# Kernel optimization log

Hardware: AMD Instinct MI355X
Metric: run time of the kernel (lower is better)

The kernel has to match this reference:

```python
import jax, jax.numpy as jnp
import numpy as np

B, N, K, E, H, V = 128, 256, 4, 300, 150, 32000  # batch, nodes/tree, max children, embed, hidden, vocab
DELTA = 1.0


def setup_inputs() -> dict:
    key = jax.random.key(0)
    ks = jax.random.split(key, 8)
    query = jax.random.randint(ks[0], (B, N), 0, V, dtype=jnp.int32)
    pos = jax.random.randint(ks[1], (B, N), 0, V, dtype=jnp.int32)
    neg = jax.random.randint(ks[2], (B, N), 0, V, dtype=jnp.int32)
    # Complete K-ary tree over N nodes: children of node t are {K*t+1, ..., K*t+K} < N; root = node 0.
    ch = np.full((N, K), -1, dtype=np.int32)
    for t in range(N):
        for j in range(K):
            c = K * t + 1 + j
            if c < N:
                ch[t, j] = c
    children = jnp.asarray(ch)
    emb = jax.random.normal(ks[3], (V, E), dtype=jnp.float32) * 0.02
    W_iou = jax.random.normal(ks[4], (E, 3 * H), dtype=jnp.float32) * 0.05
    U_iou = jax.random.normal(ks[5], (H, 3 * H), dtype=jnp.float32) * 0.05
    b_iou = jnp.zeros((3 * H,), jnp.float32)
    W_f = jax.random.normal(ks[6], (E, H), dtype=jnp.float32) * 0.05
    U_f = jax.random.normal(ks[7], (H, H), dtype=jnp.float32) * 0.05
    b_f = jnp.zeros((H,), jnp.float32)
    return {"query": query, "pos": pos, "neg": neg, "children": children,
            "emb": emb, "W_iou": W_iou, "U_iou": U_iou, "b_iou": b_iou,
            "W_f": W_f, "U_f": U_f, "b_f": b_f}


def _childsum_treelstm(x, children, W_iou, U_iou, b_iou, W_f, U_f, b_f):
    """x: [B, N, E] node embeddings. Returns root (c, h): each [B, H]."""
    Bn, Nn, _ = x.shape
    Hh = U_f.shape[0]
    h0 = jnp.zeros((Bn, Nn, Hh), x.dtype)
    c0 = jnp.zeros((Bn, Nn, Hh), x.dtype)

    def step(carry, t):
        h_all, c_all = carry
        ch = children[t]                        # [K] child indices, -1 = padding
        mask = (ch >= 0)
        idx = jnp.where(mask, ch, 0)
        m = mask.astype(x.dtype)[None, :, None]  # [1, K, 1]
        h_k = h_all[:, idx] * m                 # [B, K, H]
        c_k = c_all[:, idx] * m
        h_sum = h_k.sum(axis=1)                 # child-sum h_tilde [B, H]
        x_t = x[:, t]                           # [B, E]
        iou = x_t @ W_iou + h_sum @ U_iou + b_iou
        i, o, u = jnp.split(iou, 3, axis=-1)
        i = jax.nn.sigmoid(i)
        o = jax.nn.sigmoid(o)
        u = jnp.tanh(u)
        # per-child forget gates: f_jk = sigmoid(W_f x_j + U_f h_k + b_f)
        f = jax.nn.sigmoid((x_t @ W_f + b_f)[:, None, :] + h_k @ U_f)  # [B, K, H]
        c_t = i * u + (f * c_k).sum(axis=1)     # c_k already masked
        h_t = o * jnp.tanh(c_t)
        return (h_all.at[:, t].set(h_t), c_all.at[:, t].set(c_t)), None

    # children have larger indices than parents -> process N-1 .. 0 (root last)
    (h_all, c_all), _ = jax.lax.scan(step, (h0, c0), jnp.arange(Nn - 1, -1, -1))
    return c_all[:, 0], h_all[:, 0]


def _cosine(a, b):
    num = (a * b).sum(-1)
    den = jnp.sqrt((a * a).sum(-1) * (b * b).sum(-1)) + 1e-8
    return num / den


def reference(query, pos, neg, children, emb, W_iou, U_iou, b_iou, W_f, U_f, b_f):
    qc, _ = _childsum_treelstm(emb[query], children, W_iou, U_iou, b_iou, W_f, U_f, b_f)
    pc, _ = _childsum_treelstm(emb[pos], children, W_iou, U_iou, b_iou, W_f, U_f, b_f)
    nc, _ = _childsum_treelstm(emb[neg], children, W_iou, U_iou, b_iou, W_f, U_f, b_f)
    a = _cosine(qc, pc)  # [B]
    b = _cosine(qc, nc)  # [B]
    return jax.nn.relu(DELTA - a + b)
```

## Files before the change

### kernel.cpp

```cpp
#include <hip/hip_runtime.h>
#include <hip/hip_bf16.h>

typedef short short8 __attribute__((ext_vector_type(8)));
typedef float floatx4 __attribute__((ext_vector_type(4)));
typedef unsigned short ushort;

#define Bb 128
#define Nn 256
#define Hh 150
#define HK 160
#define Vv 32000
#define NROW 384
#define NINT 64
#define ZROW (Vv + NROW * NINT)

__device__ __forceinline__ float sigf(float x) { return 1.0f / (1.0f + __expf(-x)); }
__device__ __forceinline__ float tanhf_(float x) { return 1.0f - 2.0f / (__expf(2.0f * x) + 1.0f); }
__device__ __forceinline__ float bf2f(ushort s) { union { float f; unsigned u; } v; v.u = ((unsigned)s) << 16; return v.f; }
__device__ __forceinline__ ushort f2bf(float f) { __hip_bfloat16 h = __float2bfloat16(f); return *(ushort*)&h; }

__global__ __launch_bounds__(256) void k_prep(
    const float* __restrict__ W_iou, const float* __restrict__ W_f,
    const float* __restrict__ U_iou, const float* __restrict__ U_f,
    const float* __restrict__ b_iou, const float* __restrict__ b_f,
    short* __restrict__ Wt, short* __restrict__ Uti, short* __restrict__ Utf,
    float* __restrict__ biasw, ushort* __restrict__ h_u, float* __restrict__ c_u)
{
    int idx = blockIdx.x * 256 + threadIdx.x;
    const int nWt = 640 * 320, nUi = 464 * 160, nUf = 160 * 160;
    if (idx < nWt) {
        int n = idx / 320, k = idx % 320;
        int seg = n / 160, cc = n % 160;
        float v = 0.f;
        if (k < 300 && cc < 150) {
            if (seg == 0)      v = W_iou[k * 450 + cc];
            else if (seg == 1) v = W_iou[k * 450 + 150 + cc];
            else if (seg == 2) v = W_iou[k * 450 + 300 + cc];
            else               v = W_f[k * 150 + cc];
        }
        Wt[idx] = (short)f2bf(v);
    } else if (idx < nWt + nUi) {
        int i2 = idx - nWt; int n = i2 / 160, k = i2 % 160;
        float v = (k < 150 && n < 450) ? U_iou[k * 450 + n] : 0.f;
        Uti[i2] = (short)f2bf(v);
    } else if (idx < nWt + nUi + nUf) {
        int i2 = idx - nWt - nUi; int n = i2 / 160, k = i2 % 160;
        float v = (k < 150) ? U_f[k * 150 + n] : 0.f;
        Utf[i2] = (short)f2bf(v);
    } else if (idx < nWt + nUi + nUf + 640) {
        int n = idx - nWt - nUi - nUf;
        int seg = n / 160, cc = n % 160;
        biasw[n] = (cc < 150) ? (seg < 3 ? b_iou[seg * 150 + cc] : b_f[cc]) : 0.f;
    } else if (idx < nWt + nUi + nUf + 640 + HK) {
        int k = idx - (nWt + nUi + nUf + 640);
        h_u[(long)ZROW * HK + k] = 0;
        c_u[(long)ZROW * HK + k] = 0.f;
    }
}

__global__ __launch_bounds__(256) void k_vproj(
    const float* __restrict__ emb, const short* __restrict__ Wt,
    const float* __restrict__ biasw, ushort* __restrict__ proj,
    ushort* __restrict__ h_u, float* __restrict__ c_u)
{
    __shared__ __align__(16) short As[32 * 328];
    __shared__ __align__(16) float Tc[4][32][20];
    __shared__ __align__(16) ushort Th[4][32][24];
    const int tid = threadIdx.x;
    const int v0 = blockIdx.x * 32;

    for (int i = tid; i < 32 * 80; i += 256) {
        int r = i / 80, q = i % 80, k0 = q * 4;
        short4 sv;
        if (k0 < 300) {
            float4 x = *(const float4*)(emb + (long)(v0 + r) * 300 + k0);
            sv.x = (short)f2bf(x.x); sv.y = (short)f2bf(x.y);
            sv.z = (short)f2bf(x.z); sv.w = (short)f2bf(x.w);
        } else sv = make_short4(0, 0, 0, 0);
        *(short4*)&As[r * 328 + k0] = sv;
    }
    __syncthreads();

    const int w = tid >> 6, lane = tid & 63;
    const int m = lane & 15, quad = lane >> 4, kq = quad * 8;

    short8 a0[10], a1[10];
    #pragma unroll
    for (int ks = 0; ks < 10; ks++) {
        a0[ks] = *(const short8*)&As[m * 328 + kq + ks * 32];
        a1[ks] = *(const short8*)&As[(16 + m) * 328 + kq + ks * 32];
    }

    for (int j = w; j < 10; j += 4) {
        int col = j * 16 + m;
        const short* bp = Wt + (long)col * 320 + kq;
        floatx4 acc[4][2];
        #pragma unroll
        for (int s = 0; s < 4; s++) { acc[s][0] = {0.f,0.f,0.f,0.f}; acc[s][1] = {0.f,0.f,0.f,0.f}; }
        #pragma unroll
        for (int ks = 0; ks < 10; ks++) {
            short8 b0 = *(const short8*)(bp + 0 * 160 * 320 + ks * 32);
            short8 b1 = *(const short8*)(bp + 1 * 160 * 320 + ks * 32);
            short8 b2 = *(const short8*)(bp + 2 * 160 * 320 + ks * 32);
            short8 b3 = *(const short8*)(bp + 3 * 160 * 320 + ks * 32);
            acc[0][0] = __builtin_amdgcn_mfma_f32_16x16x32_bf16(a0[ks], b0, acc[0][0], 0, 0, 0);
            acc[0][1] = __builtin_amdgcn_mfma_f32_16x16x32_bf16(a1[ks], b0, acc[0][1], 0, 0, 0);
            acc[1][0] = __builtin_amdgcn_mfma_f32_16x16x32_bf16(a0[ks], b1, acc[1][0], 0, 0, 0);
            acc[1][1] = __builtin_amdgcn_mfma_f32_16x16x32_bf16(a1[ks], b1, acc[1][1], 0, 0, 0);
            acc[2][0] = __builtin_amdgcn_mfma_f32_16x16x32_bf16(a0[ks], b2, acc[2][0], 0, 0, 0);
            acc[2][1] = __builtin_amdgcn_mfma_f32_16x16x32_bf16(a1[ks], b2, acc[2][1], 0, 0, 0);
            acc[3][0] = __builtin_amdgcn_mfma_f32_16x16x32_bf16(a0[ks], b3, acc[3][0], 0, 0, 0);
            acc[3][1] = __builtin_amdgcn_mfma_f32_16x16x32_bf16(a1[ks], b3, acc[3][1], 0, 0, 0);
        }

        float bias[4] = { biasw[col], biasw[160 + col], biasw[320 + col], biasw[480 + col] };
        float pre[4][2][4];
        #pragma unroll
        for (int s = 0; s < 4; s++)
            #pragma unroll
            for (int g = 0; g < 2; g++)
                #pragma unroll
                for (int reg = 0; reg < 4; reg++)
                    pre[s][g][reg] = acc[s][g][reg] + bias[s];

        long tbase = (long)(blockIdx.x * 10 + j) * 2048;
        #pragma unroll
        for (int s = 0; s < 4; s++)
            #pragma unroll
            for (int g = 0; g < 2; g++) {
                unsigned u0 = (unsigned)f2bf(pre[s][g][0]) | ((unsigned)f2bf(pre[s][g][1]) << 16);
                unsigned u1 = (unsigned)f2bf(pre[s][g][2]) | ((unsigned)f2bf(pre[s][g][3]) << 16);
                *(uint2*)(proj + tbase + s * 512 + g * 256 + lane * 4) = make_uint2(u0, u1);
            }

        #pragma unroll
        for (int g = 0; g < 2; g++)
            #pragma unroll
            for (int reg = 0; reg < 4; reg++) {
                float iv = sigf(pre[0][g][reg]);
                float ov = sigf(pre[1][g][reg]);
                float uv = tanhf_(pre[2][g][reg]);
                float cc = iv * uv;
                int rr = g * 16 + quad * 4 + reg;
                Tc[w][rr][m] = cc;
                Th[w][rr][m] = f2bf(ov * tanhf_(cc));
            }
        asm volatile("s_waitcnt lgkmcnt(0)" ::: "memory");
        {
            int row = lane >> 1, half = lane & 1;
            int4 hv = *(const int4*)&Th[w][row][half * 8];
            *(int4*)(h_u + (long)(v0 + row) * HK + j * 16 + half * 8) = hv;
            #pragma unroll
            for (int qq = half; qq < 4; qq += 2) {
                float4 cv4 = *(const float4*)&Tc[w][row][qq * 4];
                *(float4*)(c_u + (long)(v0 + row) * HK + j * 16 + qq * 4) = cv4;
            }
        }
        asm volatile("s_waitcnt lgkmcnt(0)" ::: "memory");
    }
}

__global__ __launch_bounds__(256) void k_level(
    int t0, int G,
    const int* __restrict__ tq, const int* __restrict__ tp, const int* __restrict__ tn,
    const int* __restrict__ children, const ushort* __restrict__ proj,
    const short* __restrict__ Uti, const short* __restrict__ Utf,
    ushort* __restrict__ h_u, float* __restrict__ c_u)
{
    __shared__ __align__(16) short As[5][16][168];
    __shared__ int idx_s[16][4];
    __shared__ int tok_s[16];

    const int tid = threadIdx.x;
    const int gi = blockIdx.x % G;
    const int rest = blockIdx.x / G;
    const int t = t0 + rest / 24;
    const int r0 = (rest % 24) * 16;

    if (tid < 64) {
        int r = tid >> 2, j = tid & 3;
        int rg = r0 + r, g = rg >> 7, b = rg & 127;
        const int* tok = (g == 0) ? tq : (g == 1 ? tp : tn);
        int ch = children[t * 4 + j];
        int idx;
        if (ch < 0)        idx = ZROW;
        else if (ch >= 64) idx = tok[b * Nn + ch];
        else               idx = Vv + rg * NINT + ch;
        idx_s[r][j] = idx;
        if (j == 0) tok_s[r] = tok[b * Nn + t];
    }
    __syncthreads();

    for (int i = tid; i < 16 * 20; i += 256) {
        int r = i / 20, k0 = (i % 20) * 8;
        int4 v0 = *(const int4*)(h_u + (long)idx_s[r][0] * HK + k0);
        int4 v1 = *(const int4*)(h_u + (long)idx_s[r][1] * HK + k0);
        int4 v2 = *(const int4*)(h_u + (long)idx_s[r][2] * HK + k0);
        int4 v3 = *(const int4*)(h_u + (long)idx_s[r][3] * HK + k0);
        *(int4*)&As[1][r][k0] = v0;
        *(int4*)&As[2][r][k0] = v1;
        *(int4*)&As[3][r][k0] = v2;
        *(int4*)&As[4][r][k0] = v3;
        ushort s[8];
        const ushort* p0 = (const ushort*)&v0; const ushort* p1 = (const ushort*)&v1;
        const ushort* p2 = (const ushort*)&v2; const ushort* p3 = (const ushort*)&v3;
        #pragma unroll
        for (int e = 0; e < 8; e++)
            s[e] = f2bf(bf2f(p0[e]) + bf2f(p1[e]) + bf2f(p2[e]) + bf2f(p3[e]));
        *(int4*)&As[0][r][k0] = *(int4*)s;
    }
    __syncthreads();

    const int w = tid >> 6, lane = tid & 63;
    const int m = lane & 15, kq = (lane >> 4) * 8;
    const int rbase = (lane >> 4) * 4;

    for (int nt = gi * 4 + w; nt < 10; nt += 4 * G) {
        int col = nt * 16 + m;
        const short* bi  = Uti + (long)(col) * HK + kq;
        const short* bo  = Uti + (long)(150 + col) * HK + kq;
        const short* bu  = Uti + (long)(300 + col) * HK + kq;
        const short* bff = Utf + (long)col * HK + kq;
        floatx4 ai = {0.f,0.f,0.f,0.f}, ao = ai, au = ai;
        floatx4 af0 = ai, af1 = ai, af2 = ai, af3 = ai;
        #pragma unroll
        for (int ks = 0; ks < 5; ks++) {
            short8 asum = *(const short8*)&As[0][m][kq + ks * 32];
            short8 ac0  = *(const short8*)&As[1][m][kq + ks * 32];
            short8 ac1  = *(const short8*)&As[2][m][kq + ks * 32];
            short8 ac2  = *(const short8*)&As[3][m][kq + ks * 32];
            short8 ac3  = *(const short8*)&As[4][m][kq + ks * 32];
            short8 vbi = *(const short8*)(bi + ks * 32);
            short8 vbo = *(const short8*)(bo + ks * 32);
            short8 vbu = *(const short8*)(bu + ks * 32);
            short8 vbf = *(const short8*)(bff + ks * 32);
            ai  = __builtin_amdgcn_mfma_f32_16x16x32_bf16(asum, vbi, ai, 0, 0, 0);
            ao  = __builtin_amdgcn_mfma_f32_16x16x32_bf16(asum, vbo, ao, 0, 0, 0);
            au  = __builtin_amdgcn_mfma_f32_16x16x32_bf16(asum, vbu, au, 0, 0, 0);
            af0 = __builtin_amdgcn_mfma_f32_16x16x32_bf16(ac0,  vbf, af0, 0, 0, 0);
            af1 = __builtin_amdgcn_mfma_f32_16x16x32_bf16(ac1,  vbf, af1, 0, 0, 0);
            af2 = __builtin_amdgcn_mfma_f32_16x16x32_bf16(ac2,  vbf, af2, 0, 0, 0);
            af3 = __builtin_amdgcn_mfma_f32_16x16x32_bf16(ac3,  vbf, af3, 0, 0, 0);
        }

        if (col < Hh) {
            #pragma unroll
            for (int reg = 0; reg < 4; reg++) {
                int rg = r0 + rbase + reg;
                int v = tok_s[rbase + reg];
                int vb = v >> 5, rr = v & 31;
                const ushort* pb = proj + ((long)(vb * 10 + nt)) * 2048
                                 + (rr >> 4) * 256 + (((rr >> 2) & 3) * 16 + m) * 4 + (rr & 3);
                float iv = sigf(bf2f(pb[0])      + ai[reg]);
                float ov = sigf(bf2f(pb[512])    + ao[reg]);
                float uv = tanhf_(bf2f(pb[1024]) + au[reg]);
                float fpre = bf2f(pb[1536]);
                float cv = iv * uv;
                cv = fmaf(sigf(fpre + af0[reg]), c_u[(long)idx_s[rbase + reg][0] * HK + col], cv);
                cv = fmaf(sigf(fpre + af1[reg]), c_u[(long)idx_s[rbase + reg][1] * HK + col], cv);
                cv = fmaf(sigf(fpre + af2[reg]), c_u[(long)idx_s[rbase + reg][2] * HK + col], cv);
                cv = fmaf(sigf(fpre + af3[reg]), c_u[(long)idx_s[rbase + reg][3] * HK + col], cv);
                long o = (long)(Vv + rg * NINT + t) * HK + col;
                c_u[o] = cv;
                h_u[o] = f2bf(ov * tanhf_(cv));
            }
        } else {
            #pragma unroll
            for (int reg = 0; reg < 4; reg++) {
                long o = (long)(Vv + (r0 + rbase + reg) * NINT + t) * HK + col;
                c_u[o] = 0.f; h_u[o] = 0;
            }
        }
    }
}

__global__ __launch_bounds__(64) void k_cos(const float* __restrict__ c_u, float* __restrict__ out)
{
    int b = blockIdx.x, tid = threadIdx.x;
    const float* qc = c_u + (long)(Vv + (0 * Bb + b) * NINT) * HK;
    const float* pc = c_u + (long)(Vv + (1 * Bb + b) * NINT) * HK;
    const float* nc = c_u + (long)(Vv + (2 * Bb + b) * NINT) * HK;
    float qp = 0, qn = 0, qq = 0, pp = 0, nn2 = 0;
    for (int k = tid; k < Hh; k += 64) {
        float qv = qc[k], pv = pc[k], nv = nc[k];
        qp += qv * pv; qn += qv * nv; qq += qv * qv; pp += pv * pv; nn2 += nv * nv;
    }
    #pragma unroll
    for (int off = 32; off > 0; off >>= 1) {
        qp += __shfl_down(qp, off, 64);
        qn += __shfl_down(qn, off, 64);
        qq += __shfl_down(qq, off, 64);
        pp += __shfl_down(pp, off, 64);
        nn2 += __shfl_down(nn2, off, 64);
    }
    if (tid == 0) {
        float a = qp / (sqrtf(qq * pp) + 1e-8f);
        float d = qn / (sqrtf(qq * nn2) + 1e-8f);
        out[b] = fmaxf(0.0f, 1.0f - a + d);
    }
}

extern "C" void kernel_launch(void* const* d_in, const int* in_sizes, int n_in,
                              void* d_out, int out_size, void* d_ws, size_t ws_size,
                              hipStream_t stream)
{
    const int*   tq       = (const int*)d_in[0];
    const int*   tp       = (const int*)d_in[1];
    const int*   tn       = (const int*)d_in[2];
    const int*   children = (const int*)d_in[3];
    const float* emb      = (const float*)d_in[4];
    const float* W_iou    = (const float*)d_in[5];
    const float* U_iou    = (const float*)d_in[6];
    const float* b_iou    = (const float*)d_in[7];
    const float* W_f      = (const float*)d_in[8];
    const float* U_f      = (const float*)d_in[9];
    const float* b_f      = (const float*)d_in[10];
    float* out = (float*)d_out;

    char* ws = (char*)d_ws;
    ushort* proj  = (ushort*)ws;
    ushort* h_u   = (ushort*)(ws + 40960000);
    float*  c_u   = (float*)(ws + 59064640);
    short*  Wt    = (short*)(ws + 95273920);
    short*  Uti   = (short*)(ws + 95683520);
    short*  Utf   = (short*)(ws + 95832000);
    float*  biasw = (float*)(ws + 95883200);

    k_prep<<<1194, 256, 0, stream>>>(W_iou, W_f, U_iou, U_f, b_iou, b_f,
                                     Wt, Uti, Utf, biasw, h_u, c_u);
    k_vproj<<<Vv / 32, 256, 0, stream>>>(emb, Wt, biasw, proj, h_u, c_u);
    k_level<<<43 * 24 * 1, 256, 0, stream>>>(21, 1, tq, tp, tn, children, proj, Uti, Utf, h_u, c_u);
    k_level<<<16 * 24 * 2, 256, 0, stream>>>(5,  2, tq, tp, tn, children, proj, Uti, Utf, h_u, c_u);
    k_level<<<4 * 24 * 3, 256, 0, stream>>>(1,   3, tq, tp, tn, children, proj, Uti, Utf, h_u, c_u);
    k_level<<<1 * 24 * 3, 256, 0, stream>>>(0,   3, tq, tp, tn, children, proj, Uti, Utf, h_u, c_u);
    k_cos<<<Bb, 64, 0, stream>>>(c_u, out);
}
```

Measured before the change: 292.8 us.

## Row-major projection layout and stage child cell states in shared memory

Changes the vocab projection table from an MFMA-fragment tiled layout to a row-major [token][640] layout, written through shared memory so stores are coalesced 16-byte rows. The level kernel then reads each token's gate pre-activations contiguously. It also prefetches the four children's cell states into shared memory with vectorized float4 loads, replacing scattered per-element global loads in the epilogue. This adds about 42KB of LDS per block, which may reduce occupancy, plus an extra barrier in the projection kernel.

Result: faster. 274.2 us (-6.3%).

```diff
diff --git a/kernel.cpp b/kernel.cpp
--- a/kernel.cpp
+++ b/kernel.cpp
@@ -11,6 +11,7 @@
 #define HK 160
 #define Vv 32000
 #define NROW 384
+#define PROJC 640
 #define NINT 64
 #define ZROW (Vv + NROW * NINT)
 
@@ -66,6 +67,8 @@
     __shared__ __align__(16) short As[32 * 328];
     __shared__ __align__(16) float Tc[4][32][20];
     __shared__ __align__(16) ushort Th[4][32][24];
+    ushort (*Tp)[32][72] = (ushort (*)[32][72])As;
+
     const int tid = threadIdx.x;
     const int v0 = blockIdx.x * 32;
 
@@ -90,6 +93,7 @@
         a0[ks] = *(const short8*)&As[m * 328 + kq + ks * 32];
         a1[ks] = *(const short8*)&As[(16 + m) * 328 + kq + ks * 32];
     }
+    __syncthreads();
 
     for (int j = w; j < 10; j += 4) {
         int col = j * 16 + m;
@@ -123,37 +127,39 @@
                 for (int reg = 0; reg < 4; reg++)
                     pre[s][g][reg] = acc[s][g][reg] + bias[s];
 
-        long tbase = (long)(blockIdx.x * 10 + j) * 2048;
-        #pragma unroll
-        for (int s = 0; s < 4; s++)
-            #pragma unroll
-            for (int g = 0; g < 2; g++) {
-                unsigned u0 = (unsigned)f2bf(pre[s][g][0]) | ((unsigned)f2bf(pre[s][g][1]) << 16);
-                unsigned u1 = (unsigned)f2bf(pre[s][g][2]) | ((unsigned)f2bf(pre[s][g][3]) << 16);
-                *(uint2*)(proj + tbase + s * 512 + g * 256 + lane * 4) = make_uint2(u0, u1);
-            }
-
         #pragma unroll
         for (int g = 0; g < 2; g++)
             #pragma unroll
             for (int reg = 0; reg < 4; reg++) {
+                int rr = g * 16 + quad * 4 + reg;
+                #pragma unroll
+                for (int s = 0; s < 4; s++)
+                    Tp[w][rr][s * 16 + m] = f2bf(pre[s][g][reg]);
                 float iv = sigf(pre[0][g][reg]);
                 float ov = sigf(pre[1][g][reg]);
                 float uv = tanhf_(pre[2][g][reg]);
                 float cc = iv * uv;
-                int rr = g * 16 + quad * 4 + reg;
                 Tc[w][rr][m] = cc;
                 Th[w][rr][m] = f2bf(ov * tanhf_(cc));
             }
         asm volatile("s_waitcnt lgkmcnt(0)" ::: "memory");
         {
             int row = lane >> 1, half = lane & 1;
+            long rowv = v0 + row;
+            #pragma unroll
+            for (int s2 = 0; s2 < 2; s2++) {
+                int s = half * 2 + s2;
+                int4 p0 = *(const int4*)&Tp[w][row][s * 16];
+                int4 p1 = *(const int4*)&Tp[w][row][s * 16 + 8];
+                *(int4*)(proj + rowv * PROJC + s * 160 + j * 16)     = p0;
+                *(int4*)(proj + rowv * PROJC + s * 160 + j * 16 + 8) = p1;
+            }
             int4 hv = *(const int4*)&Th[w][row][half * 8];
-            *(int4*)(h_u + (long)(v0 + row) * HK + j * 16 + half * 8) = hv;
+            *(int4*)(h_u + rowv * HK + j * 16 + half * 8) = hv;
             #pragma unroll
             for (int qq = half; qq < 4; qq += 2) {
                 float4 cv4 = *(const float4*)&Tc[w][row][qq * 4];
-                *(float4*)(c_u + (long)(v0 + row) * HK + j * 16 + qq * 4) = cv4;
+                *(float4*)(c_u + rowv * HK + j * 16 + qq * 4) = cv4;
             }
         }
         asm volatile("s_waitcnt lgkmcnt(0)" ::: "memory");
@@ -168,6 +174,7 @@
     ushort* __restrict__ h_u, float* __restrict__ c_u)
 {
     __shared__ __align__(16) short As[5][16][168];
+    __shared__ __align__(16) float Cs[4][16][164];
     __shared__ int idx_s[16][4];
     __shared__ int tok_s[16];
 
@@ -208,6 +215,12 @@
         for (int e = 0; e < 8; e++)
             s[e] = f2bf(bf2f(p0[e]) + bf2f(p1[e]) + bf2f(p2[e]) + bf2f(p3[e]));
         *(int4*)&As[0][r][k0] = *(int4*)s;
+    }
+    for (int i = tid; i < 16 * 40; i += 256) {
+        int r = i / 40, k0 = (i % 40) * 4;
+        #pragma unroll
+        for (int j = 0; j < 4; j++)
+            *(float4*)&Cs[j][r][k0] = *(const float4*)(c_u + (long)idx_s[r][j] * HK + k0);
     }
     __syncthreads();
 
@@ -246,20 +259,17 @@
         if (col < Hh) {
             #pragma unroll
             for (int reg = 0; reg < 4; reg++) {
-                int rg = r0 + rbase + reg;
-                int v = tok_s[rbase + reg];
-                int vb = v >> 5, rr = v & 31;
-                const ushort* pb = proj + ((long)(vb * 10 + nt)) * 2048
-                                 + (rr >> 4) * 256 + (((rr >> 2) & 3) * 16 + m) * 4 + (rr & 3);
-                float iv = sigf(bf2f(pb[0])      + ai[reg]);
-                float ov = sigf(bf2f(pb[512])    + ao[reg]);
-                float uv = tanhf_(bf2f(pb[1024]) + au[reg]);
-                float fpre = bf2f(pb[1536]);
+                int r = rbase + reg, rg = r0 + r;
+                const ushort* pr = proj + (long)tok_s[r] * PROJC;
+                float iv = sigf(bf2f(pr[col])        + ai[reg]);
+                float ov = sigf(bf2f(pr[160 + col])  + ao[reg]);
+                float uv = tanhf_(bf2f(pr[320 + col]) + au[reg]);
+                float fpre = bf2f(pr[480 + col]);
                 float cv = iv * uv;
-                cv = fmaf(sigf(fpre + af0[reg]), c_u[(long)idx_s[rbase + reg][0] * HK + col], cv);
-                cv = fmaf(sigf(fpre + af1[reg]), c_u[(long)idx_s[rbase + reg][1] * HK + col], cv);
-                cv = fmaf(sigf(fpre + af2[reg]), c_u[(long)idx_s[rbase + reg][2] * HK + col], cv);
-                cv = fmaf(sigf(fpre + af3[reg]), c_u[(long)idx_s[rbase + reg][3] * HK + col], cv);
+                cv = fmaf(sigf(fpre + af0[reg]), Cs[0][r][col], cv);
+                cv = fmaf(sigf(fpre + af1[reg]), Cs[1][r][col], cv);
+                cv = fmaf(sigf(fpre + af2[reg]), Cs[2][r][col], cv);
+                cv = fmaf(sigf(fpre + af3[reg]), Cs[3][r][col], cv);
                 long o = (long)(Vv + rg * NINT + t) * HK + col;
                 c_u[o] = cv;
                 h_u[o] = f2bf(ov * tanhf_(cv));
```
